# Optimization experiments

Hardware: AMD Instinct MI355X
Metric: run time of the kernel (lower is better)

## Reference

```python
import jax, jax.numpy as jnp
import numpy as np

B, T, C = 4, 2048, 2048
N_HEAD = 16
HEAD_DIM = C // N_HEAD
ROPE_BASE = 10000.0


def setup_inputs() -> dict:
    key = jax.random.key(0)
    k1, k2, k3 = jax.random.split(key, 3)
    x = jax.random.normal(k1, (B, T, C), dtype=jnp.float32)
    Wqkv = jax.random.normal(k2, (C, 3 * C), dtype=jnp.float32) * 0.02
    bqkv = jnp.zeros((3 * C,), dtype=jnp.float32)
    Wproj = jax.random.normal(k3, (C, C), dtype=jnp.float32) * 0.02
    bproj = jnp.zeros((C,), dtype=jnp.float32)
    return {"x": x, "Wqkv": Wqkv, "bqkv": bqkv, "Wproj": Wproj, "bproj": bproj}


def _rope_cos_sin(seq_len, head_dim, dtype):
    inv_freq = 1.0 / (ROPE_BASE ** (jnp.arange(0, head_dim, 2, dtype=jnp.float32) / head_dim))
    t = jnp.arange(seq_len, dtype=jnp.float32)
    freqs = jnp.einsum("i,j->ij", t, inv_freq)          # [T, D/2]
    emb = jnp.concatenate([freqs, freqs], axis=-1)       # [T, D]
    return jnp.cos(emb).astype(dtype), jnp.sin(emb).astype(dtype)


def _rotate_half(x):
    half = x.shape[-1] // 2
    x1, x2 = x[..., :half], x[..., half:]
    return jnp.concatenate([-x2, x1], axis=-1)


def reference(x, Wqkv, bqkv, Wproj, bproj):
    b, t, c = x.shape
    qkv = x @ Wqkv + bqkv                                # [B, T, 3C]
    q, k, v = jnp.split(qkv, 3, axis=-1)
    # [B, T, C] -> [B, H, T, D]
    def to_heads(u):
        return u.reshape(b, t, N_HEAD, HEAD_DIM).transpose(0, 2, 1, 3)
    q, k, v = to_heads(q), to_heads(k), to_heads(v)
    cos, sin = _rope_cos_sin(t, HEAD_DIM, x.dtype)       # [T, D]
    cos = cos[None, None]                                # [1, 1, T, D]
    sin = sin[None, None]
    q = q * cos + _rotate_half(q) * sin
    k = k * cos + _rotate_half(k) * sin
    scale = 1.0 / np.sqrt(HEAD_DIM).astype(np.float32)
    scores = jnp.einsum("bhqd,bhkd->bhqk", q, k) * scale  # [B, H, T, T]
    causal = jnp.tril(jnp.ones((t, t), dtype=bool))
    scores = jnp.where(causal[None, None], scores, jnp.finfo(scores.dtype).min)
    att = jax.nn.softmax(scores, axis=-1)
    y = jnp.einsum("bhqk,bhkd->bhqd", att, v)             # [B, H, T, D]
    y = y.transpose(0, 2, 1, 3).reshape(b, t, c)
    return y @ Wproj + bproj
```

## Files before the change

kernel.cpp:

```cpp
#include <hip/hip_runtime.h>
#include <hip/hip_bf16.h>
#include <stdint.h>
#include <math.h>

#define NB 4
#define NT 2048
#define NC 2048
#define NH 16
#define HD 128
#define BT (NB*NT)

typedef __attribute__((ext_vector_type(8))) short s16x8;
typedef __attribute__((ext_vector_type(4))) short s16x4;
typedef __attribute__((ext_vector_type(4))) float f32x4;

typedef __attribute__((address_space(1))) void as1_void;
typedef __attribute__((address_space(3))) void as3_void;

static __device__ __forceinline__ unsigned short f2bf(float f) {
  union { float f; uint32_t u; } v; v.f = f;
  return (unsigned short)((v.u + 0x7fffu + ((v.u >> 16) & 1u)) >> 16);
}
static __device__ __forceinline__ float bf2f(unsigned short u) {
  union { uint32_t u; float f; } v; v.u = ((uint32_t)u) << 16;
  return v.f;
}
static __device__ __forceinline__ void async16(unsigned short* lds, const unsigned short* g) {
  __builtin_amdgcn_global_load_lds((as1_void*)g, (as3_void*)lds, 16, 0, 0);
}
static __device__ __forceinline__ uint32_t lds_off(void* p) {
  return (uint32_t)(size_t)(as3_void*)p;
}

__global__ void k_convert_bf16(const float* __restrict__ in, unsigned short* __restrict__ out, int n8) {
  int i = blockIdx.x * blockDim.x + threadIdx.x;
  if (i >= n8) return;
  const float4* p = (const float4*)in + (size_t)i * 2;
  float4 a = p[0], b = p[1];
  union { unsigned short s[8]; uint4 u; } o;
  o.s[0] = f2bf(a.x); o.s[1] = f2bf(a.y); o.s[2] = f2bf(a.z); o.s[3] = f2bf(a.w);
  o.s[4] = f2bf(b.x); o.s[5] = f2bf(b.y); o.s[6] = f2bf(b.z); o.s[7] = f2bf(b.w);
  ((uint4*)out)[i] = o.u;
}

__global__ void k_transpose_bf16(const float* __restrict__ W, unsigned short* __restrict__ WT, int K, int N) {
  __shared__ unsigned short tile[64][65];
  const int k0 = blockIdx.y * 64, n0 = blockIdx.x * 64;
  const int t = threadIdx.x;
  const int jj = t & 63, base_i = t >> 6;
  #pragma unroll
  for (int p = 0; p < 16; ++p) {
    int i = p * 4 + base_i;
    tile[i][jj] = f2bf(W[(size_t)(k0 + i) * N + n0 + jj]);
  }
  __syncthreads();
  #pragma unroll
  for (int p = 0; p < 16; ++p) {
    int j = p * 4 + base_i;
    WT[(size_t)(n0 + j) * K + k0 + jj] = tile[jj][j];
  }
}

__global__ void k_rope(unsigned short* __restrict__ Q, unsigned short* __restrict__ Kb) {
  int idx = blockIdx.x * 256 + threadIdx.x;
  int d = idx & 63;
  int tpos = (idx >> 6) & (NT - 1);
  int bh = idx >> 17;
  size_t o = ((size_t)bh * NT + tpos) * HD + d;
  float invf = exp2f(-(float)d * 0.2076205059304602f);
  float ang = (float)tpos * invf;
  float s, c;
  sincosf(ang, &s, &c);
  float q1 = bf2f(Q[o]),  q2 = bf2f(Q[o + 64]);
  float k1 = bf2f(Kb[o]), k2 = bf2f(Kb[o + 64]);
  const float qs = 0.08838834764831845f * 1.4426950408889634f;
  Q[o]       = f2bf((q1 * c - q2 * s) * qs);
  Q[o + 64]  = f2bf((q2 * c + q1 * s) * qs);
  Kb[o]      = f2bf(k1 * c - k2 * s);
  Kb[o + 64] = f2bf(k2 * c + k1 * s);
}

template<int MODE>
__global__ __launch_bounds__(512, 2)
void k_gemm256(const unsigned short* __restrict__ A,
               const unsigned short* __restrict__ Bt,
               const float* __restrict__ bias,
               float* __restrict__ OutF,
               unsigned short* __restrict__ Qd,
               unsigned short* __restrict__ Kd,
               unsigned short* __restrict__ Vd,
               int M, int N, int K)
{
  __shared__ __align__(16) unsigned short Al[2][256 * 64];
  __shared__ __align__(16) unsigned short Bl[2][256 * 64];
  const int t = threadIdx.x;
  const int l = t & 63;
  const int wv = t >> 6;
  const int wm = wv >> 2, wn = wv & 3;
  const int bm = blockIdx.y * 256, bn = blockIdx.x * 256;
  const int lr = l & 15, lg = l >> 4;

  f32x4 acc[8][4];
  #pragma unroll
  for (int i = 0; i < 8; ++i)
    #pragma unroll
    for (int j = 0; j < 4; ++j)
      acc[i][j] = f32x4{0.f, 0.f, 0.f, 0.f};

  const int ubase = (t & 448) * 8;

  auto stage = [&](int buf, int k0) {
    #pragma unroll
    for (int i = 0; i < 4; ++i) {
      const int Cc = i * 512 + t;
      const int row = Cc >> 3;
      const int kc = (Cc & 7) ^ (row & 7);
      async16(&Al[buf][(i * 512) * 8 + ubase], &A[(size_t)(bm + row) * K + k0 + kc * 8]);
      async16(&Bl[buf][(i * 512) * 8 + ubase], &Bt[(size_t)(bn + row) * K + k0 + kc * 8]);
    }
  };

  auto compute = [&](int buf) {
    #pragma unroll
    for (int kk = 0; kk < 2; ++kk) {
      s16x8 af[8], bfr[4];
      #pragma unroll
      for (int mi = 0; mi < 8; ++mi) {
        const int row = wm * 128 + mi * 16 + lr;
        const int ch = (kk * 4 + lg) ^ (row & 7);
        af[mi] = *(const s16x8*)&Al[buf][row * 64 + ch * 8];
      }
      #pragma unroll
      for (int ni = 0; ni < 4; ++ni) {
        const int row = wn * 64 + ni * 16 + lr;
        const int ch = (kk * 4 + lg) ^ (row & 7);
        bfr[ni] = *(const s16x8*)&Bl[buf][row * 64 + ch * 8];
      }
      __builtin_amdgcn_s_setprio(1);
      #pragma unroll
      for (int mi = 0; mi < 8; ++mi)
        #pragma unroll
        for (int ni = 0; ni < 4; ++ni)
          acc[mi][ni] = __builtin_amdgcn_mfma_f32_16x16x32_bf16(af[mi], bfr[ni], acc[mi][ni], 0, 0, 0);
      __builtin_amdgcn_s_setprio(0);
    }
  };

  stage(0, 0);
  const int nkt = K >> 6;
  int cur = 0;
  #pragma unroll 1
  for (int tt = 0; tt < nkt - 1; ++tt) {
    stage(cur ^ 1, (tt + 1) << 6);
    asm volatile("s_waitcnt vmcnt(8)" ::: "memory");
    __builtin_amdgcn_s_barrier();
    compute(cur);
    __builtin_amdgcn_s_barrier();
    cur ^= 1;
  }
  asm volatile("s_waitcnt vmcnt(0)" ::: "memory");
  __builtin_amdgcn_s_barrier();
  compute(cur);

  #pragma unroll
  for (int mi = 0; mi < 8; ++mi) {
    #pragma unroll
    for (int ni = 0; ni < 4; ++ni) {
      const int col = bn + wn * 64 + ni * 16 + lr;
      const float bv = bias[col];
      #pragma unroll
      for (int r = 0; r < 4; ++r) {
        const int row = bm + wm * 128 + mi * 16 + lg * 4 + r;
        const float v = acc[mi][ni][r] + bv;
        if (MODE == 1) {
          OutF[(size_t)row * N + col] = v;
        } else {
          const int which = col >> 11;
          const int cc = col & 2047;
          const int h = cc >> 7, d = cc & 127;
          const int b = row >> 11, tp = row & 2047;
          unsigned short* dst = (which == 0) ? Qd : (which == 1 ? Kd : Vd);
          dst[(((size_t)(b * NH + h)) * NT + tp) * HD + d] = f2bf(v);
        }
      }
    }
  }
}

__global__ __launch_bounds__(256, 2)
void k_attn(const unsigned short* __restrict__ Q,
            const unsigned short* __restrict__ Kg,
            const unsigned short* __restrict__ Vg,
            unsigned short* __restrict__ Yatt)
{
  __shared__ __align__(16) unsigned short Kl[64 * 128];
  __shared__ __align__(16) unsigned short Vl[64 * 128];
  const int bh = blockIdx.x;
  const int pair = blockIdx.y;
  const int b = bh >> 4, h = bh & 15;
  const int t = threadIdx.x, l = t & 63, wv = t >> 6;
  const int lr = l & 15, lg = l >> 4;
  const size_t hoff = (size_t)bh * NT * HD;
  const unsigned short* Qh = Q + hoff;
  const unsigned short* Kh = Kg + hoff;
  const unsigned short* Vh = Vg + hoff;
  const uint32_t vbase = lds_off(Vl);

  #pragma unroll 1
  for (int rep = 0; rep < 2; ++rep) {
    const int qb = rep ? (31 - pair) : pair;
    const int q0w = qb * 64 + wv * 16;
    const int qrow = q0w + lr;

    s16x8 qf[4];
    #pragma unroll
    for (int m = 0; m < 4; ++m)
      qf[m] = *(const s16x8*)(Qh + (size_t)qrow * HD + m * 32 + lg * 8);

    f32x4 yt[8];
    #pragma unroll
    for (int n = 0; n < 8; ++n) yt[n] = f32x4{0.f, 0.f, 0.f, 0.f};
    float mrun = -1e30f, lrun = 0.f;

    const int nkv = qb + 1;
    for (int kv = 0; kv < nkv; ++kv) {
      const int kv0 = kv * 64;
      #pragma unroll
      for (int i = 0; i < 4; ++i) {
        const int Cc = i * 256 + t;
        {
          const int krow = Cc >> 4;
          const int kc = (Cc & 15) ^ (krow & 7);
          async16(&Kl[(i * 256 + (t & 192)) * 8], &Kh[(size_t)(kv0 + krow) * HD + kc * 8]);
        }
        {
          const int S = Cc >> 3, c8 = Cc & 7;
          const int kq = S >> 3, dq = S & 7;
          const int vk = kq * 4 + (c8 >> 1), vd = dq * 16 + (c8 & 1) * 8;
          async16(&Vl[(i * 256 + (t & 192)) * 8], &Vh[(size_t)(kv0 + vk) * HD + vd]);
        }
      }
      __syncthreads();

      f32x4 st[4];
      __builtin_amdgcn_s_setprio(1);
      #pragma unroll
      for (int kt = 0; kt < 4; ++kt) {
        f32x4 a = f32x4{0.f, 0.f, 0.f, 0.f};
        const int krow = kt * 16 + lr;
        #pragma unroll
        for (int m = 0; m < 4; ++m) {
          const int ch = (m * 4 + lg) ^ (krow & 7);
          s16x8 kf = *(const s16x8*)&Kl[krow * 128 + ch * 8];
          a = __builtin_amdgcn_mfma_f32_16x16x32_bf16(kf, qf[m], a, 0, 0, 0);
        }
        st[kt] = a;
      }
      __builtin_amdgcn_s_setprio(0);

      if (kv0 + 63 > q0w) {
        #pragma unroll
        for (int kt = 0; kt < 4; ++kt)
          #pragma unroll
          for (int r = 0; r < 4; ++r) {
            const int key = kv0 + kt * 16 + lg * 4 + r;
            if (key > qrow) st[kt][r] = -3.0e38f;
          }
      }

      float tm = -3.0e38f;
      #pragma unroll
      for (int kt = 0; kt < 4; ++kt)
        #pragma unroll
        for (int r = 0; r < 4; ++r) tm = fmaxf(tm, st[kt][r]);
      tm = fmaxf(tm, __shfl_xor(tm, 16));
      tm = fmaxf(tm, __shfl_xor(tm, 32));
      const float mnew = fmaxf(mrun, tm);
      const float fsc = exp2f(mrun - mnew);
      mrun = mnew;
      lrun *= fsc;
      #pragma unroll
      for (int n = 0; n < 8; ++n)
        #pragma unroll
        for (int r = 0; r < 4; ++r) yt[n][r] *= fsc;

      unsigned short pb[16];
      float psum = 0.f;
      #pragma unroll
      for (int kt = 0; kt < 4; ++kt)
        #pragma unroll
        for (int r = 0; r < 4; ++r) {
          const float p = exp2f(st[kt][r] - mnew);
          psum += p;
          pb[kt * 4 + r] = f2bf(p);
        }
      lrun += psum;

      s16x8 pf[2];
      #pragma unroll
      for (int gk = 0; gk < 2; ++gk)
        #pragma unroll
        for (int j = 0; j < 8; ++j)
          pf[gk][j] = (short)pb[(gk * 2 + (j >> 2)) * 4 + (j & 3)];

      #pragma unroll
      for (int gk = 0; gk < 2; ++gk) {
        s16x4 va[8], vb2[8];
        #pragma unroll
        for (int n = 0; n < 8; ++n) {
          const uint32_t a0 = vbase + ((uint32_t)((gk * 8 + lg) * 8 + n)) * 128 + (uint32_t)lr * 8;
          asm volatile("ds_read_b64_tr_b16 %0, %1" : "=v"(va[n])  : "v"(a0));
          asm volatile("ds_read_b64_tr_b16 %0, %1" : "=v"(vb2[n]) : "v"(a0 + 4096));
        }
        asm volatile("s_waitcnt lgkmcnt(0)" ::: "memory");
        __builtin_amdgcn_sched_barrier(0);
        __builtin_amdgcn_s_setprio(1);
        #pragma unroll
        for (int n = 0; n < 8; ++n) {
          s16x8 vf;
          vf[0] = va[n][0];  vf[1] = va[n][1];  vf[2] = va[n][2];  vf[3] = va[n][3];
          vf[4] = vb2[n][0]; vf[5] = vb2[n][1]; vf[6] = vb2[n][2]; vf[7] = vb2[n][3];
          yt[n] = __builtin_amdgcn_mfma_f32_16x16x32_bf16(vf, pf[gk], yt[n], 0, 0, 0);
        }
        __builtin_amdgcn_s_setprio(0);
      }
      __syncthreads();
    }

    lrun += __shfl_xor(lrun, 16);
    lrun += __shfl_xor(lrun, 32);
    const float inv = 1.f / lrun;
    unsigned short* yrow = Yatt + (size_t)(b * NT + q0w + lr) * NC + h * HD;
    #pragma unroll
    for (int n = 0; n < 8; ++n)
      #pragma unroll
      for (int r = 0; r < 4; ++r)
        yrow[n * 16 + lg * 4 + r] = f2bf(yt[n][r] * inv);
  }
}

extern "C" void kernel_launch(void* const* d_in, const int* in_sizes, int n_in,
                              void* d_out, int out_size, void* d_ws, size_t ws_size,
                              hipStream_t stream) {
  (void)in_sizes; (void)n_in; (void)out_size; (void)ws_size;
  const float* x     = (const float*)d_in[0];
  const float* Wqkv  = (const float*)d_in[1];
  const float* bqkv  = (const float*)d_in[2];
  const float* Wproj = (const float*)d_in[3];
  const float* bproj = (const float*)d_in[4];
  float* out = (float*)d_out;
  char* ws = (char*)d_ws;

  unsigned short* xb     = (unsigned short*)(ws);
  unsigned short* WqkvT  = (unsigned short*)(ws + 33554432);
  unsigned short* WprojT = (unsigned short*)(ws + 58720256);
  unsigned short* Qb     = (unsigned short*)(ws + 67108864);
  unsigned short* Kb     = (unsigned short*)(ws + 100663296);
  unsigned short* Vb     = (unsigned short*)(ws + 134217728);
  unsigned short* att    = xb;

  k_convert_bf16<<<dim3(8192), dim3(256), 0, stream>>>(x, xb, BT * NC / 8);
  k_transpose_bf16<<<dim3(96, 32), dim3(256), 0, stream>>>(Wqkv, WqkvT, NC, 3 * NC);
  k_transpose_bf16<<<dim3(32, 32), dim3(256), 0, stream>>>(Wproj, WprojT, NC, NC);
  k_gemm256<0><<<dim3(24, 32), dim3(512), 0, stream>>>(xb, WqkvT, bqkv, nullptr, Qb, Kb, Vb, BT, 3 * NC, NC);
  k_rope<<<dim3(32768), dim3(256), 0, stream>>>(Qb, Kb);
  k_attn<<<dim3(64, 16), dim3(256), 0, stream>>>(Qb, Kb, Vb, att);
  k_gemm256<1><<<dim3(8, 32), dim3(512), 0, stream>>>(att, WprojT, bproj, out, nullptr, nullptr, nullptr, BT, NC, NC);
}
```

Before: 470.8 us.

## Restructure GEMM mainloop into eight-phase interleaved load/compute pipeline

Replaces the two-stage double-buffered GEMM loop with a finer-grained schedule that splits each 64-wide K tile into two 32-wide halves. Staging of A and B sub-tiles is interleaved with half-tile MFMA blocks, separated by barriers. The LDS layout changes to pack two rows per 64-element line with a new XOR swizzle. The goal is to overlap global-to-LDS copies with MFMA work and cut the stall at each tile boundary, at the cost of more barriers per iteration. The last iteration also issues a redundant prefetch of tile 0.

```diff
diff --git a/kernel.cpp b/kernel.cpp
--- a/kernel.cpp
+++ b/kernel.cpp
@@ -16,6 +16,8 @@
 
 typedef __attribute__((address_space(1))) void as1_void;
 typedef __attribute__((address_space(3))) void as3_void;
+
+#define CFENCE asm volatile("" ::: "memory")
 
 static __device__ __forceinline__ unsigned short f2bf(float f) {
   union { float f; uint32_t u; } v; v.f = f;
@@ -82,23 +84,24 @@
 
 template<int MODE>
 __global__ __launch_bounds__(512, 2)
-void k_gemm256(const unsigned short* __restrict__ A,
-               const unsigned short* __restrict__ Bt,
-               const float* __restrict__ bias,
-               float* __restrict__ OutF,
-               unsigned short* __restrict__ Qd,
-               unsigned short* __restrict__ Kd,
-               unsigned short* __restrict__ Vd,
-               int M, int N, int K)
+void k_gemm8p(const unsigned short* __restrict__ A,
+              const unsigned short* __restrict__ Bt,
+              const float* __restrict__ bias,
+              float* __restrict__ OutF,
+              unsigned short* __restrict__ Qd,
+              unsigned short* __restrict__ Kd,
+              unsigned short* __restrict__ Vd,
+              int M, int N, int K)
 {
-  __shared__ __align__(16) unsigned short Al[2][256 * 64];
-  __shared__ __align__(16) unsigned short Bl[2][256 * 64];
+  __shared__ __align__(16) unsigned short Al[2][2][8192];
+  __shared__ __align__(16) unsigned short Bl[2][2][8192];
   const int t = threadIdx.x;
   const int l = t & 63;
   const int wv = t >> 6;
   const int wm = wv >> 2, wn = wv & 3;
   const int bm = blockIdx.y * 256, bn = blockIdx.x * 256;
   const int lr = l & 15, lg = l >> 4;
+  const int wbase = (t & 448);
 
   f32x4 acc[8][4];
   #pragma unroll
@@ -107,60 +110,102 @@
     for (int j = 0; j < 4; ++j)
       acc[i][j] = f32x4{0.f, 0.f, 0.f, 0.f};
 
-  const int ubase = (t & 448) * 8;
-
-  auto stage = [&](int buf, int k0) {
-    #pragma unroll
-    for (int i = 0; i < 4; ++i) {
-      const int Cc = i * 512 + t;
-      const int row = Cc >> 3;
-      const int kc = (Cc & 7) ^ (row & 7);
-      async16(&Al[buf][(i * 512) * 8 + ubase], &A[(size_t)(bm + row) * K + k0 + kc * 8]);
-      async16(&Bl[buf][(i * 512) * 8 + ubase], &Bt[(size_t)(bn + row) * K + k0 + kc * 8]);
-    }
+  int srow0, sc0, srow1, sc1;
+  {
+    int n = t;            int lq = n >> 3, v = (n & 7) ^ (lq & 7);
+    srow0 = 2 * lq + (v >> 2); sc0 = v & 3;
+  }
+  {
+    int n = 512 + t;      int lq = n >> 3, v = (n & 7) ^ (lq & 7);
+    srow1 = 2 * lq + (v >> 2); sc1 = v & 3;
+  }
+
+  auto stageA = [&](int buf, int kk, int k0) {
+    async16(&Al[buf][kk][(0 * 512 + wbase) * 8], &A[(size_t)(bm + srow0) * K + k0 + kk * 32 + sc0 * 8]);
+    async16(&Al[buf][kk][(1 * 512 + wbase) * 8], &A[(size_t)(bm + srow1) * K + k0 + kk * 32 + sc1 * 8]);
   };
-
-  auto compute = [&](int buf) {
-    #pragma unroll
-    for (int kk = 0; kk < 2; ++kk) {
-      s16x8 af[8], bfr[4];
-      #pragma unroll
-      for (int mi = 0; mi < 8; ++mi) {
-        const int row = wm * 128 + mi * 16 + lr;
-        const int ch = (kk * 4 + lg) ^ (row & 7);
-        af[mi] = *(const s16x8*)&Al[buf][row * 64 + ch * 8];
-      }
-      #pragma unroll
-      for (int ni = 0; ni < 4; ++ni) {
-        const int row = wn * 64 + ni * 16 + lr;
-        const int ch = (kk * 4 + lg) ^ (row & 7);
-        bfr[ni] = *(const s16x8*)&Bl[buf][row * 64 + ch * 8];
-      }
-      __builtin_amdgcn_s_setprio(1);
-      #pragma unroll
-      for (int mi = 0; mi < 8; ++mi)
-        #pragma unroll
-        for (int ni = 0; ni < 4; ++ni)
-          acc[mi][ni] = __builtin_amdgcn_mfma_f32_16x16x32_bf16(af[mi], bfr[ni], acc[mi][ni], 0, 0, 0);
-      __builtin_amdgcn_s_setprio(0);
-    }
+  auto stageB = [&](int buf, int kk, int k0) {
+    async16(&Bl[buf][kk][(0 * 512 + wbase) * 8], &Bt[(size_t)(bn + srow0) * K + k0 + kk * 32 + sc0 * 8]);
+    async16(&Bl[buf][kk][(1 * 512 + wbase) * 8], &Bt[(size_t)(bn + srow1) * K + k0 + kk * 32 + sc1 * 8]);
   };
-
-  stage(0, 0);
+  auto lda = [&](int buf, int kk, int mi) -> s16x8 {
+    const int row = wm * 128 + mi * 16 + lr;
+    const int lq = row >> 1;
+    const int phys = (((row & 1) << 2) | lg) ^ (lq & 7);
+    return *(const s16x8*)&Al[buf][kk][lq * 64 + phys * 8];
+  };
+  auto ldb = [&](int buf, int kk, int ni) -> s16x8 {
+    const int row = wn * 64 + ni * 16 + lr;
+    const int lq = row >> 1;
+    const int phys = (((row & 1) << 2) | lg) ^ (lq & 7);
+    return *(const s16x8*)&Bl[buf][kk][lq * 64 + phys * 8];
+  };
+
+  stageA(0, 0, 0); stageB(0, 0, 0); stageA(0, 1, 0); stageB(0, 1, 0);
+  asm volatile("s_waitcnt vmcnt(4)" ::: "memory");
+  CFENCE; __builtin_amdgcn_s_barrier(); CFENCE;
+
   const int nkt = K >> 6;
-  int cur = 0;
   #pragma unroll 1
-  for (int tt = 0; tt < nkt - 1; ++tt) {
-    stage(cur ^ 1, (tt + 1) << 6);
-    asm volatile("s_waitcnt vmcnt(8)" ::: "memory");
-    __builtin_amdgcn_s_barrier();
-    compute(cur);
-    __builtin_amdgcn_s_barrier();
-    cur ^= 1;
-  }
-  asm volatile("s_waitcnt vmcnt(0)" ::: "memory");
-  __builtin_amdgcn_s_barrier();
-  compute(cur);
+  for (int tau = 0; tau < nkt; ++tau) {
+    const int buf = tau & 1, nbuf = buf ^ 1;
+    const int k0n = (tau + 1 < nkt) ? ((tau + 1) << 6) : 0;
+    s16x8 af[4], bfr[4];
+
+    stageA(nbuf, 0, k0n);
+    #pragma unroll
+    for (int i = 0; i < 4; ++i) af[i] = lda(buf, 0, i);
+    #pragma unroll
+    for (int j = 0; j < 4; ++j) bfr[j] = ldb(buf, 0, j);
+    __builtin_amdgcn_s_setprio(1);
+    #pragma unroll
+    for (int i = 0; i < 4; ++i)
+      #pragma unroll
+      for (int j = 0; j < 4; ++j)
+        acc[i][j] = __builtin_amdgcn_mfma_f32_16x16x32_bf16(af[i], bfr[j], acc[i][j], 0, 0, 0);
+    __builtin_amdgcn_s_setprio(0);
+    CFENCE; __builtin_amdgcn_s_barrier(); CFENCE;
+
+    stageB(nbuf, 0, k0n);
+    #pragma unroll
+    for (int i = 0; i < 4; ++i) af[i] = lda(buf, 0, 4 + i);
+    __builtin_amdgcn_s_setprio(1);
+    #pragma unroll
+    for (int i = 0; i < 4; ++i)
+      #pragma unroll
+      for (int j = 0; j < 4; ++j)
+        acc[4 + i][j] = __builtin_amdgcn_mfma_f32_16x16x32_bf16(af[i], bfr[j], acc[4 + i][j], 0, 0, 0);
+    __builtin_amdgcn_s_setprio(0);
+    asm volatile("s_waitcnt vmcnt(4)" ::: "memory");
+    CFENCE; __builtin_amdgcn_s_barrier(); CFENCE;
+
+    stageA(nbuf, 1, k0n);
+    #pragma unroll
+    for (int i = 0; i < 4; ++i) af[i] = lda(buf, 1, i);
+    #pragma unroll
+    for (int j = 0; j < 4; ++j) bfr[j] = ldb(buf, 1, j);
+    __builtin_amdgcn_s_setprio(1);
+    #pragma unroll
+    for (int i = 0; i < 4; ++i)
+      #pragma unroll
+      for (int j = 0; j < 4; ++j)
+        acc[i][j] = __builtin_amdgcn_mfma_f32_16x16x32_bf16(af[i], bfr[j], acc[i][j], 0, 0, 0);
+    __builtin_amdgcn_s_setprio(0);
+    CFENCE; __builtin_amdgcn_s_barrier(); CFENCE;
+
+    stageB(nbuf, 1, k0n);
+    #pragma unroll
+    for (int i = 0; i < 4; ++i) af[i] = lda(buf, 1, 4 + i);
+    __builtin_amdgcn_s_setprio(1);
+    #pragma unroll
+    for (int i = 0; i < 4; ++i)
+      #pragma unroll
+      for (int j = 0; j < 4; ++j)
+        acc[4 + i][j] = __builtin_amdgcn_mfma_f32_16x16x32_bf16(af[i], bfr[j], acc[4 + i][j], 0, 0, 0);
+    __builtin_amdgcn_s_setprio(0);
+    asm volatile("s_waitcnt vmcnt(4)" ::: "memory");
+    CFENCE; __builtin_amdgcn_s_barrier(); CFENCE;
+  }
 
   #pragma unroll
   for (int mi = 0; mi < 8; ++mi) {
@@ -362,8 +407,8 @@
   k_convert_bf16<<<dim3(8192), dim3(256), 0, stream>>>(x, xb, BT * NC / 8);
   k_transpose_bf16<<<dim3(96, 32), dim3(256), 0, stream>>>(Wqkv, WqkvT, NC, 3 * NC);
   k_transpose_bf16<<<dim3(32, 32), dim3(256), 0, stream>>>(Wproj, WprojT, NC, NC);
-  k_gemm256<0><<<dim3(24, 32), dim3(512), 0, stream>>>(xb, WqkvT, bqkv, nullptr, Qb, Kb, Vb, BT, 3 * NC, NC);
+  k_gemm8p<0><<<dim3(24, 32), dim3(512), 0, stream>>>(xb, WqkvT, bqkv, nullptr, Qb, Kb, Vb, BT, 3 * NC, NC);
   k_rope<<<dim3(32768), dim3(256), 0, stream>>>(Qb, Kb);
   k_attn<<<dim3(64, 16), dim3(256), 0, stream>>>(Qb, Kb, Vb, att);
-  k_gemm256<1><<<dim3(8, 32), dim3(512), 0, stream>>>(att, WprojT, bproj, out, nullptr, nullptr, nullptr, BT, NC, NC);
-}
+  k_gemm8p<1><<<dim3(8, 32), dim3(512), 0, stream>>>(att, WprojT, bproj, out, nullptr, nullptr, nullptr, BT, NC, NC);
+}
```

Measured after the change: 468.2 us. Within noise of the previous version (-0.6%).
